# Kernel tuning notes

Hardware: AMD Instinct MI355X
Metric: run time of the kernel (lower is better)

Reference implementation:

```python
import jax, jax.numpy as jnp
import numpy as np
from jax import lax

B, T, C, H, W = 2, 1, 128, 128, 128
NH, WS, K = 4, 8, 16          # heads, search window, top-k
HD = C // NH                  # head dim
OFF = WS // 2                 # window top-left offset


def setup_inputs() -> dict:
    key = jax.random.key(0)
    ks = jax.random.split(key, 16)
    def p(k, shape, fan):
        return jax.random.normal(k, shape, jnp.float32) / np.float32(np.sqrt(fan))
    inp = {"vid": jax.random.normal(ks[0], (B, T, C, H, W), jnp.float32)}
    for i, n in enumerate(["q", "k", "v"]):
        inp[n + "_dw_w"] = p(ks[1 + 4 * i], (C, 1, 3, 3), 9)
        inp[n + "_dw_b"] = jnp.zeros((C,), jnp.float32)
        inp[n + "_pw_w"] = p(ks[3 + 4 * i], (C, C), C)
        inp[n + "_pw_b"] = jnp.zeros((C,), jnp.float32)
    inp["proj_w"] = p(ks[13], (C, C), C)
    inp["proj_b"] = jnp.zeros((C,), jnp.float32)
    return inp


def reflect(i, L):
    # dnls reflect bounds: -1 -> 1, L -> L-2
    return jnp.where(i < 0, -i, jnp.where(i >= L, 2 * (L - 1) - i, i))


def sep_conv(x, dw_w, dw_b, pw_w, pw_b):
    # SepConv2d: depthwise 3x3 (+bias) -> ReLU -> pointwise 1x1 (+bias)
    y = lax.conv_general_dilated(x, dw_w, (1, 1), [(1, 1), (1, 1)],
                                 feature_group_count=x.shape[1],
                                 dimension_numbers=("NCHW", "OIHW", "NCHW"))
    y = jax.nn.relu(y + dw_b[None, :, None, None])
    return jnp.einsum("nchw,oc->nohw", y, pw_w) + pw_b[None, :, None, None]


def forward(vid, q_dw_w, q_dw_b, q_pw_w, q_pw_b, k_dw_w, k_dw_b, k_pw_w, k_pw_b,
            v_dw_w, v_dw_b, v_pw_w, v_pw_b, proj_w, proj_b):
    scale = jnp.float32(HD ** -0.5)
    x = vid.reshape(B * T, C, H, W)
    q = sep_conv(x, q_dw_w, q_dw_b, q_pw_w, q_pw_b) * scale
    k = sep_conv(x, k_dw_w, k_dw_b, k_pw_w, k_pw_b)
    v = sep_conv(x, v_dw_w, v_dw_b, v_pw_w, v_pw_b)
    q = q.reshape(B, T, NH, HD, H, W)
    k = k.reshape(B, T, NH, HD, H, W)
    v = v.reshape(B, T, NH, HD, H, W)

    # windowed product search: 64 candidates per query, reflect bounds
    d = jnp.arange(WS) - OFF                              # offsets -4..3
    hidx = reflect(jnp.arange(H)[None, :] + d[:, None], H)  # [WS, H]
    widx = reflect(jnp.arange(W)[None, :] + d[:, None], W)  # [WS, W]
    dlist = []
    for i in range(WS):  # loop over fixed dy offsets (structural, size 8)
        kh = k[..., hidx[i], :]               # shift rows: [B,T,NH,HD,H,W]
        kd = kh[..., widx]                    # [B,T,NH,HD,H,WS,W]
        dlist.append(jnp.einsum("btnchw,btnchxw->btnhwx", q, kd))
    dists = jnp.stack(dlist, axis=-2).reshape(B, T, NH, H, W, WS * WS)

    # top-k + softmax over neighbors
    dk, ik = lax.top_k(dists, K)              # [B,T,NH,H,W,K]
    wgt = jax.nn.softmax(dk, axis=-1)

    # decode flat candidate index -> absolute (reflected) pixel coords
    oy = ik // WS - OFF
    ox = ik % WS - OFF
    hh = reflect(jnp.arange(H)[:, None, None] + oy, H)
    ww = reflect(jnp.arange(W)[:, None] + ox, W)
    flat = (hh * W + ww).reshape(B, T, NH, 1, H * W * K)

    # weighted patch (pixel) sum aggregation per head
    v2 = v.reshape(B, T, NH, HD, H * W)
    g = jnp.take_along_axis(v2, flat, axis=-1).reshape(B, T, NH, HD, H, W, K)
    out = jnp.einsum("btnchwk,btnhwk->btnchw", g, wgt)
    out = out.reshape(B, T, C, H, W)          # head-major channels == '(h c)'

    # proj linear over channels; fold with ps=1,stride0=1 is exact identity/zvid=1
    tok = out.transpose(0, 1, 3, 4, 2)        # [B,T,H,W,C]
    tok = tok @ proj_w.T + proj_b
    return tok.transpose(0, 1, 4, 2, 3)       # [B,T,C,H,W]


def reference(vid, q_dw_w, q_dw_b, q_pw_w, q_pw_b, k_dw_w, k_dw_b, k_pw_w, k_pw_b,
              v_dw_w, v_dw_b, v_pw_w, v_pw_b, proj_w, proj_b):
    return forward(vid, q_dw_w, q_dw_b, q_pw_w, q_pw_b, k_dw_w, k_dw_b, k_pw_w,
                   k_pw_b, v_dw_w, v_dw_b, v_pw_w, v_pw_b, proj_w, proj_b)
```

## Files before the change

kernel.cpp:

```cpp
#include <hip/hip_runtime.h>
#include <hip/hip_fp16.h>

static constexpr int Wd  = 128;
static constexpr int Hd  = 128;
static constexpr int HWc = Wd * Hd;
static constexpr int Cc  = 128;
static constexpr int NHc = 4;
static constexpr int Bc  = 2;

__device__ __forceinline__ int refl(int i, int L) {
    i = i < 0 ? -i : i;
    return i >= L ? 2 * (L - 1) - i : i;
}

__device__ __forceinline__ unsigned f2s(float f) {
    unsigned u = __float_as_uint(f);
    return u ^ (0x80000000u | (unsigned)((int)u >> 31));
}
__device__ __forceinline__ float s2f(unsigned s) {
    unsigned u = (s & 0x80000000u) ? (s ^ 0x80000000u) : ~s;
    return __uint_as_float(u);
}

__device__ __forceinline__ unsigned f2bf(float f) {
    unsigned u = __float_as_uint(f);
    u += 0x7fffu + ((u >> 16) & 1u);
    return u >> 16;
}


__global__ __launch_bounds__(256) void dw3_kernel(
    const float* __restrict__ vid,
    const float* __restrict__ wq, const float* __restrict__ bq,
    const float* __restrict__ wk, const float* __restrict__ bk,
    const float* __restrict__ wv, const float* __restrict__ bv,
    float* __restrict__ yq, float* __restrict__ yk, float* __restrict__ yv)
{
    int bid = blockIdx.x;
    int bxd = bid & 63;
    int bc  = bid >> 6;
    int bx  = ((bxd & 7) << 3) | (bxd >> 3);
    int pix = bx * 256 + threadIdx.x;
    int c   = bc & (Cc - 1);
    int y = pix >> 7, x = pix & (Wd - 1);
    const float* src = vid + bc * HWc;
    const float* wpq = wq + c * 9;
    const float* wpk = wk + c * 9;
    const float* wpv = wv + c * 9;
    float aq = 0.f, ak = 0.f, av = 0.f;
    #pragma unroll
    for (int ky = 0; ky < 3; ++ky) {
        int iy = y + ky - 1;
        if (iy < 0 || iy >= Hd) continue;
        #pragma unroll
        for (int kx = 0; kx < 3; ++kx) {
            int ix = x + kx - 1;
            if (ix < 0 || ix >= Wd) continue;
            float v = src[iy * Wd + ix];
            int k = ky * 3 + kx;
            aq = fmaf(v, wpq[k], aq);
            ak = fmaf(v, wpk[k], ak);
            av = fmaf(v, wpv[k], av);
        }
    }
    int o = bc * HWc + pix;
    yq[o] = fmaxf(aq + bq[c], 0.f);
    yk[o] = fmaxf(ak + bk[c], 0.f);
    yv[o] = fmaxf(av + bv[c], 0.f);
}

__global__ __launch_bounds__(256) void pw_kernel(
    const float* y0p, const float* y1p, const float* y2p,
    const float* __restrict__ w0,  const float* __restrict__ w1,  const float* __restrict__ w2,
    const float* __restrict__ b0,  const float* __restrict__ b1,  const float* __restrict__ b2,
    float* o0, float* o1, float* o2,
    float scale0)
{
    extern __shared__ float lds[];
    float* wl = lds;
    float* yl = lds + 8448;

    int bidl = blockIdx.x;
    int z    = bidl >> 9;
    int bxd  = bidl & 511;
    int bx   = (bxd & 256) | ((bxd & 7) << 5) | ((bxd >> 3) & 31);
    const float* yin  = z == 0 ? y0p : (z == 1 ? y1p : y2p);
    const float* wmat = z == 0 ? w0  : (z == 1 ? w1  : w2);
    const float* bias = z == 0 ? b0  : (z == 1 ? b1  : b2);
    float* out        = z == 0 ? o0  : (z == 1 ? o1  : o2);
    float scale       = z == 0 ? scale0 : 1.f;

    int tid = threadIdx.x;
    int ot = tid & 15, pt = tid >> 4;
    int gp  = bx * 64;
    int b   = gp >> 14;
    int pof = gp & (HWc - 1);
    const float* yb = yin + b * Cc * HWc + pof;

    float acc[2][4][4];
    #pragma unroll
    for (int a = 0; a < 2; ++a)
        #pragma unroll
        for (int i = 0; i < 4; ++i)
            #pragma unroll
            for (int j = 0; j < 4; ++j) acc[a][i][j] = 0.f;

    for (int kh = 0; kh < 2; ++kh) {
        int c0 = kh * 64;
        for (int i = tid; i < 8192; i += 256) {
            int cc = i & 63, o = i >> 6;
            wl[cc * 132 + o] = wmat[o * 128 + c0 + cc];
        }
        for (int i = tid; i < 4096; i += 256) {
            int p = i & 63, cc = i >> 6;
            yl[cc * 68 + p] = yb[(c0 + cc) * HWc + p];
        }
        __syncthreads();
        #pragma unroll 4
        for (int cc = 0; cc < 64; ++cc) {
            float4 wv[2];
            wv[0] = *(const float4*)(wl + cc * 132 + 4 * ot);
            wv[1] = *(const float4*)(wl + cc * 132 + 64 + 4 * ot);
            const float4 pv = *(const float4*)(yl + cc * 68 + 4 * pt);
            const float pp[4] = {pv.x, pv.y, pv.z, pv.w};
            #pragma unroll
            for (int oh = 0; oh < 2; ++oh) {
                const float wo[4] = {wv[oh].x, wv[oh].y, wv[oh].z, wv[oh].w};
                #pragma unroll
                for (int oi = 0; oi < 4; ++oi)
                    #pragma unroll
                    for (int pi = 0; pi < 4; ++pi)
                        acc[oh][oi][pi] = fmaf(wo[oi], pp[pi], acc[oh][oi][pi]);
            }
        }
        __syncthreads();
    }

    float* ob = out + b * Cc * HWc + pof;
    #pragma unroll
    for (int oh = 0; oh < 2; ++oh)
        #pragma unroll
        for (int oi = 0; oi < 4; ++oi) {
            int o = oh * 64 + 4 * ot + oi;
            float bo = bias[o];
            float4 v;
            v.x = (acc[oh][oi][0] + bo) * scale;
            v.y = (acc[oh][oi][1] + bo) * scale;
            v.z = (acc[oh][oi][2] + bo) * scale;
            v.w = (acc[oh][oi][3] + bo) * scale;
            *(float4*)(ob + o * HWc + 4 * pt) = v;
        }
}

__global__ __launch_bounds__(512) void attn_kernel(
    const float* q, const float* __restrict__ kk,
    const float* __restrict__ vv, float* att)
{
    extern __shared__ float alds[];
    float* kreg       = alds;
    unsigned* vreg    = (unsigned*)(alds + 7200);
    float* q_l        = alds + 7200 + 3600;
    int tid = threadIdx.x;
    int bid = blockIdx.x;
    int band = bid & 7;
    int r    = bid >> 3;
    int ty = (band << 1) | (r & 1);
    int tx = (r >> 1) & 15;
    int bn = (r >> 5) & 7;
    int x0 = tx * 8, y0 = ty * 8;
    const float* kb = kk + bn * 32 * HWc;
    const float* vb = vv + bn * 32 * HWc;

    int qq = tid & 7;
    int pl = tid >> 3;
    int px = pl & 7, py = pl >> 3;
    int gq = (y0 + py) * Wd + (x0 + px);

    {
        int cb = tid & 7;
        const float* kc = kb + cb * 4 * HWc;
        const float* vc = vb + cb * 4 * HWc;
        float* kq    = kreg + cb * 900;
        unsigned* vq = vreg + cb * 450;
        for (int u = tid; u < 1800; u += 512) {
            int pix = u >> 3;
            int ry = pix / 15, rx = pix - ry * 15;
            int go = refl(y0 - 4 + ry, Hd) * Wd + refl(x0 - 4 + rx, Wd);
            float4 a, b;
            a.x = kc[go];
            a.y = kc[HWc + go];
            a.z = kc[2 * HWc + go];
            a.w = kc[3 * HWc + go];
            b.x = vc[go];
            b.y = vc[HWc + go];
            b.z = vc[2 * HWc + go];
            b.w = vc[3 * HWc + go];
            *(float4*)(kq + pix * 4) = a;
            uint2 pk;
            pk.x = f2bf(b.x) | (f2bf(b.y) << 16);
            pk.y = f2bf(b.z) | (f2bf(b.w) << 16);
            *(uint2*)(vq + pix * 2) = pk;
        }
        const float* qb = q + bn * 32 * HWc;
        for (int u = tid; u < 2048; u += 512) {
            int c = u >> 6, pix = u & 63;
            q_l[pix * 36 + c] = qb[c * HWc + (y0 + (pix >> 3)) * Wd + x0 + (pix & 7)];
        }
    }
    __syncthreads();

    float d[8];
    #pragma unroll
    for (int i = 0; i < 8; ++i) d[i] = 0.f;
    {
        int base_p = (py + qq) * 15 + px;
        const float* myq = q_l + pl * 36;
        #pragma unroll
        for (int cq = 0; cq < 8; ++cq) {
            const float4 q4 = *(const float4*)(myq + cq * 4);
            const float* rq = kreg + cq * 900 + base_p * 4;
            #pragma unroll
            for (int j = 0; j < 8; ++j) {
                const float4 kv = *(const float4*)(rq + j * 4);
                d[j] = fmaf(q4.x, kv.x, fmaf(q4.y, kv.y, fmaf(q4.z, kv.z, fmaf(q4.w, kv.w, d[j]))));
            }
        }
    }
    unsigned s[8];
    #pragma unroll
    for (int i = 0; i < 8; ++i) s[i] = f2s(d[i]);

    unsigned rkc[8];
    #pragma unroll
    for (int i = 0; i < 8; ++i) rkc[i] = 0u;
    #pragma unroll
    for (int i = 0; i < 7; ++i) {
        #pragma unroll
        for (int j = i + 1; j < 8; ++j) {
            rkc[i] += (unsigned)(s[j] > s[i]);
            rkc[j] += (unsigned)(s[i] >= s[j]);
        }
    }
    #pragma unroll
    for (int m = 1; m <= 7; ++m) {
        unsigned plow = ((m >= 4) ? (qq >> 2) : (m >= 2) ? (qq >> 1) : qq) & 1;
        #pragma unroll
        for (int j = 0; j < 8; ++j) {
            unsigned spa = __shfl_xor(s[j], m) + plow;
            #pragma unroll
            for (int i = 0; i < 8; ++i)
                rkc[i] += (unsigned)(spa > s[i]);
        }
    }

    unsigned smax = s[0];
    #pragma unroll
    for (int i = 1; i < 8; ++i) smax = max(smax, s[i]);
    smax = max(smax, (unsigned)__shfl_xor(smax, 1));
    smax = max(smax, (unsigned)__shfl_xor(smax, 2));
    smax = max(smax, (unsigned)__shfl_xor(smax, 4));
    float dmax = s2f(smax);
    float w[8];
    float sum = 0.f;
    #pragma unroll
    for (int i = 0; i < 8; ++i) {
        float e = (rkc[i] < 16u) ? __expf(s2f(s[i]) - dmax) : 0.f;
        w[i] = e;
        sum += e;
    }
    sum += __shfl_xor(sum, 1);
    sum += __shfl_xor(sum, 2);
    sum += __shfl_xor(sum, 4);
    float inv = 1.0f / sum;

    unsigned* entp = (unsigned*)(q_l + pl * 36);
    #pragma unroll
    for (int i = 0; i < 8; ++i) {
        if (rkc[i] < 16u) {
            unsigned hb = __half_as_ushort(__float2half(w[i]));
            entp[rkc[i]] = (hb << 16) | (unsigned)(qq * 8 + i);
        }
    }

    uint4 ea = *(const uint4*)(entp);
    uint4 eb = *(const uint4*)(entp + 4);
    uint4 ec = *(const uint4*)(entp + 8);
    uint4 ed = *(const uint4*)(entp + 12);
    unsigned ent[16] = {ea.x, ea.y, ea.z, ea.w, eb.x, eb.y, eb.z, eb.w,
                        ec.x, ec.y, ec.z, ec.w, ed.x, ed.y, ed.z, ed.w};
    float a0 = 0.f, a1 = 0.f, a2 = 0.f, a3 = 0.f;
    int pbase = py * 15 + px;
    const unsigned* rq = vreg + qq * 450;
    #pragma unroll
    for (int e = 0; e < 16; ++e) {
        unsigned en = ent[e];
        int tt = en & 63;
        int dy = tt >> 3, dx = tt & 7;
        float wg = __half2float(__ushort_as_half((unsigned short)(en >> 16)));
        const uint2 pv = *(const uint2*)(rq + (pbase + dy * 15 + dx) * 2);
        float v0 = __uint_as_float(pv.x << 16);
        float v1 = __uint_as_float(pv.x & 0xffff0000u);
        float v2 = __uint_as_float(pv.y << 16);
        float v3 = __uint_as_float(pv.y & 0xffff0000u);
        a0 = fmaf(wg, v0, a0);
        a1 = fmaf(wg, v1, a1);
        a2 = fmaf(wg, v2, a2);
        a3 = fmaf(wg, v3, a3);
    }

    float* op = att + (bn * 32 + qq * 4) * HWc + gq;
    op[0]       = a0 * inv;
    op[HWc]     = a1 * inv;
    op[2 * HWc] = a2 * inv;
    op[3 * HWc] = a3 * inv;
}

extern "C" void kernel_launch(void* const* d_in, const int* in_sizes, int n_in,
                              void* d_out, int out_size, void* d_ws, size_t ws_size,
                              hipStream_t stream)
{
    const float* vid  = (const float*)d_in[0];
    const float* qdww = (const float*)d_in[1];
    const float* qdwb = (const float*)d_in[2];
    const float* qpww = (const float*)d_in[3];
    const float* qpwb = (const float*)d_in[4];
    const float* kdww = (const float*)d_in[5];
    const float* kdwb = (const float*)d_in[6];
    const float* kpww = (const float*)d_in[7];
    const float* kpwb = (const float*)d_in[8];
    const float* vdww = (const float*)d_in[9];
    const float* vdwb = (const float*)d_in[10];
    const float* vpww = (const float*)d_in[11];
    const float* vpwb = (const float*)d_in[12];
    const float* pjw  = (const float*)d_in[13];
    const float* pjb  = (const float*)d_in[14];

    float* ws = (float*)d_ws;
    const size_t SZ = (size_t)Bc * Cc * HWc;
    float* buf0 = ws;
    float* buf1 = ws + SZ;
    float* buf2 = ws + 2 * SZ;

    hipFuncSetAttribute((const void*)pw_kernel,   hipFuncAttributeMaxDynamicSharedMemorySize, 51200);
    hipFuncSetAttribute((const void*)attn_kernel, hipFuncAttributeMaxDynamicSharedMemorySize, 52416);

    dw3_kernel<<<dim3(64 * Bc * Cc, 1, 1), 256, 0, stream>>>(
        vid, qdww, qdwb, kdww, kdwb, vdww, vdwb, buf0, buf1, buf2);

    const float scale = 0.17677669529663687f;
    pw_kernel<<<dim3(512 * 3, 1, 1), 256, 51200, stream>>>(
        buf0, buf1, buf2, qpww, kpww, vpww, qpwb, kpwb, vpwb, buf0, buf1, buf2, scale);

    attn_kernel<<<dim3(2048, 1, 1), 512, 52416, stream>>>(
        buf0, buf1, buf2, buf0);

    pw_kernel<<<dim3(512, 1, 1), 256, 51200, stream>>>(
        buf0, buf0, buf0, pjw, pjw, pjw, pjb, pjb, pjb, (float*)d_out, (float*)d_out, (float*)d_out, 1.f);
}
```

Before: 176.9 us.

## Fuse depthwise 3x3 conv into pointwise conv tile loading

Removes the separate depthwise conv kernel and computes the 3x3 depthwise conv plus ReLU on the fly while staging the input tile into LDS inside the pointwise kernel. This avoids writing and re-reading three full intermediate tensors. The cost is 9 global loads per staged element, hitting the cache, and scalar weight loads inside the staging loop. The staging phase becomes heavier and is not overlapped with compute.

```diff
diff --git a/kernel.cpp b/kernel.cpp
--- a/kernel.cpp
+++ b/kernel.cpp
@@ -28,53 +28,16 @@
     return u >> 16;
 }
 
-
-__global__ __launch_bounds__(256) void dw3_kernel(
+__global__ __launch_bounds__(256) void pw_kernel(
     const float* __restrict__ vid,
-    const float* __restrict__ wq, const float* __restrict__ bq,
-    const float* __restrict__ wk, const float* __restrict__ bk,
-    const float* __restrict__ wv, const float* __restrict__ bv,
-    float* __restrict__ yq, float* __restrict__ yk, float* __restrict__ yv)
-{
-    int bid = blockIdx.x;
-    int bxd = bid & 63;
-    int bc  = bid >> 6;
-    int bx  = ((bxd & 7) << 3) | (bxd >> 3);
-    int pix = bx * 256 + threadIdx.x;
-    int c   = bc & (Cc - 1);
-    int y = pix >> 7, x = pix & (Wd - 1);
-    const float* src = vid + bc * HWc;
-    const float* wpq = wq + c * 9;
-    const float* wpk = wk + c * 9;
-    const float* wpv = wv + c * 9;
-    float aq = 0.f, ak = 0.f, av = 0.f;
-    #pragma unroll
-    for (int ky = 0; ky < 3; ++ky) {
-        int iy = y + ky - 1;
-        if (iy < 0 || iy >= Hd) continue;
-        #pragma unroll
-        for (int kx = 0; kx < 3; ++kx) {
-            int ix = x + kx - 1;
-            if (ix < 0 || ix >= Wd) continue;
-            float v = src[iy * Wd + ix];
-            int k = ky * 3 + kx;
-            aq = fmaf(v, wpq[k], aq);
-            ak = fmaf(v, wpk[k], ak);
-            av = fmaf(v, wpv[k], av);
-        }
-    }
-    int o = bc * HWc + pix;
-    yq[o] = fmaxf(aq + bq[c], 0.f);
-    yk[o] = fmaxf(ak + bk[c], 0.f);
-    yv[o] = fmaxf(av + bv[c], 0.f);
-}
-
-__global__ __launch_bounds__(256) void pw_kernel(
-    const float* y0p, const float* y1p, const float* y2p,
+    const float* y0p,
+    const float* __restrict__ dw_wq, const float* __restrict__ dw_bq,
+    const float* __restrict__ dw_wk, const float* __restrict__ dw_bk,
+    const float* __restrict__ dw_wv, const float* __restrict__ dw_bv,
     const float* __restrict__ w0,  const float* __restrict__ w1,  const float* __restrict__ w2,
     const float* __restrict__ b0,  const float* __restrict__ b1,  const float* __restrict__ b2,
     float* o0, float* o1, float* o2,
-    float scale0)
+    float scale0, int fuse_dw)
 {
     extern __shared__ float lds[];
     float* wl = lds;
@@ -84,9 +47,10 @@
     int z    = bidl >> 9;
     int bxd  = bidl & 511;
     int bx   = (bxd & 256) | ((bxd & 7) << 5) | ((bxd >> 3) & 31);
-    const float* yin  = z == 0 ? y0p : (z == 1 ? y1p : y2p);
     const float* wmat = z == 0 ? w0  : (z == 1 ? w1  : w2);
     const float* bias = z == 0 ? b0  : (z == 1 ? b1  : b2);
+    const float* wdw  = z == 0 ? dw_wq : (z == 1 ? dw_wk : dw_wv);
+    const float* bdw  = z == 0 ? dw_bq : (z == 1 ? dw_bk : dw_bv);
     float* out        = z == 0 ? o0  : (z == 1 ? o1  : o2);
     float scale       = z == 0 ? scale0 : 1.f;
 
@@ -95,7 +59,8 @@
     int gp  = bx * 64;
     int b   = gp >> 14;
     int pof = gp & (HWc - 1);
-    const float* yb = yin + b * Cc * HWc + pof;
+    int yrow = pof >> 7, xcol = pof & (Wd - 1);
+    const float* yb = y0p + b * Cc * HWc + pof;
 
     float acc[2][4][4];
     #pragma unroll
@@ -111,9 +76,31 @@
             int cc = i & 63, o = i >> 6;
             wl[cc * 132 + o] = wmat[o * 128 + c0 + cc];
         }
-        for (int i = tid; i < 4096; i += 256) {
-            int p = i & 63, cc = i >> 6;
-            yl[cc * 68 + p] = yb[(c0 + cc) * HWc + p];
+        if (fuse_dw) {
+            for (int i = tid; i < 4096; i += 256) {
+                int p = i & 63, cc = i >> 6;
+                int c = c0 + cc;
+                const float* src = vid + (b * Cc + c) * HWc;
+                const float* wp9 = wdw + c * 9;
+                float a = 0.f;
+                #pragma unroll
+                for (int ky = 0; ky < 3; ++ky) {
+                    int iy = yrow + ky - 1;
+                    if (iy < 0 || iy >= Hd) continue;
+                    #pragma unroll
+                    for (int kx = 0; kx < 3; ++kx) {
+                        int ix = xcol + p + kx - 1;
+                        if (ix < 0 || ix >= Wd) continue;
+                        a = fmaf(src[iy * Wd + ix], wp9[ky * 3 + kx], a);
+                    }
+                }
+                yl[cc * 68 + p] = fmaxf(a + bdw[c], 0.f);
+            }
+        } else {
+            for (int i = tid; i < 4096; i += 256) {
+                int p = i & 63, cc = i >> 6;
+                yl[cc * 68 + p] = yb[(c0 + cc) * HWc + p];
+            }
         }
         __syncthreads();
         #pragma unroll 4
@@ -344,16 +331,16 @@
     hipFuncSetAttribute((const void*)pw_kernel,   hipFuncAttributeMaxDynamicSharedMemorySize, 51200);
     hipFuncSetAttribute((const void*)attn_kernel, hipFuncAttributeMaxDynamicSharedMemorySize, 52416);
 
-    dw3_kernel<<<dim3(64 * Bc * Cc, 1, 1), 256, 0, stream>>>(
-        vid, qdww, qdwb, kdww, kdwb, vdww, vdwb, buf0, buf1, buf2);
-
     const float scale = 0.17677669529663687f;
     pw_kernel<<<dim3(512 * 3, 1, 1), 256, 51200, stream>>>(
-        buf0, buf1, buf2, qpww, kpww, vpww, qpwb, kpwb, vpwb, buf0, buf1, buf2, scale);
+        vid, vid, qdww, qdwb, kdww, kdwb, vdww, vdwb,
+        qpww, kpww, vpww, qpwb, kpwb, vpwb, buf0, buf1, buf2, scale, 1);
 
     attn_kernel<<<dim3(2048, 1, 1), 512, 52416, stream>>>(
         buf0, buf1, buf2, buf0);
 
     pw_kernel<<<dim3(512, 1, 1), 256, 51200, stream>>>(
-        buf0, buf0, buf0, pjw, pjw, pjw, pjb, pjb, pjb, (float*)d_out, (float*)d_out, (float*)d_out, 1.f);
-}
+        vid, buf0, qdww, qdwb, kdww, kdwb, vdww, vdwb,
+        pjw, pjw, pjw, pjb, pjb, pjb,
+        (float*)d_out, (float*)d_out, (float*)d_out, 1.f, 0);
+}
```

Measured after the change: 222.6 us. 1.26x slower.
